# Optimization experiments

Measured on AMD Instinct MI355X. Metric: run time of the kernel, lower is better.

Reference implementation:

```python
import jax, jax.numpy as jnp
import numpy as np

DELTA_VAR = 0.5
DELTA_DIST = 1.5
ALPHA, BETA, GAMMA = 1.0, 1.0, 0.001
EPS = 1e-8


def setup_inputs() -> dict:
    key = jax.random.key(0)
    k1, k2 = jax.random.split(key)
    N, D, C = 4_000_000, 16, 64
    features = jax.random.normal(k1, (N, D), dtype=jnp.float32)
    labels = jax.random.randint(k2, (N,), 0, C)  # every cluster id present w.h.p.
    return {"features": features, "labels": labels, "num_clusters": C}


def _discriminative_loss(features, labels, C):
    # per-cluster counts and means (scatter-mean, replaces the boolean-mask loop)
    ones = jnp.ones(features.shape[0], dtype=features.dtype)
    counts = jax.ops.segment_sum(ones, labels, num_segments=C)            # (C,)
    sums = jax.ops.segment_sum(features, labels, num_segments=C)          # (C, D)
    safe_counts = jnp.maximum(counts, 1.0)
    means = sums / safe_counts[:, None]                                   # (C, D)

    # intra-cluster (variance) loss: mean over clusters of mean hinge^2
    dists = jnp.linalg.norm(features - means[labels] + EPS, axis=1)       # (N,)
    hinge2 = jnp.square(jnp.maximum(dists - DELTA_VAR, 0.0))
    per_cluster = jax.ops.segment_sum(hinge2, labels, num_segments=C) / safe_counts
    var_loss = jnp.mean(per_cluster)

    # inter-cluster (distance) loss over all ordered pairs i != j
    diff = means[:, None, :] - means[None, :, :] + EPS                    # (C, C, D)
    pdist = jnp.linalg.norm(diff, axis=-1)                                # (C, C)
    h = jnp.square(jnp.maximum(2.0 * DELTA_DIST - pdist, 0.0))
    h = h * (1.0 - jnp.eye(C, dtype=h.dtype))
    dist_loss = jnp.sum(h) / float(C * (C - 1))

    # regularization: mean centroid norm
    reg_loss = jnp.mean(jnp.linalg.norm(means + EPS, axis=1))

    total = ALPHA * var_loss + BETA * dist_loss + GAMMA * reg_loss
    return jnp.stack([total, var_loss, dist_loss, reg_loss])  # (4,)


def reference(features, labels, num_clusters):
    return _discriminative_loss(features, labels, num_clusters)
```

## Files before the change

kernel.cpp:

```cpp
#include <hip/hip_runtime.h>
#include <math.h>

#define C 64
#define D 16
#define EPSF 1e-8f
#define DVAR 0.5f
#define DDIST 1.5f
#define FPSCALE 65536.0f
#define INV_FPSCALE (1.0f / 65536.0f)
#define VARSCALE 4294967296.0
#define INV_VARSCALE (1.0 / 4294967296.0)

#define NB 2048
#define SLICE 1088

#define GF0 (NB * SLICE)
#define V0 (GF0 + 1088)

__global__ __launch_bounds__(256) void k_sums(const float4* __restrict__ f4,
                                              const int* __restrict__ labels, int N,
                                              int* __restrict__ arr) {
    __shared__ int s_sums[C * 17];
    __shared__ unsigned s_cnt[C];
    int t = threadIdx.x;
    int b = blockIdx.x;
    for (int i = t; i < C * 17; i += 256) s_sums[i] = 0;
    if (t < C) s_cnt[t] = 0u;
    __syncthreads();

    int ntiles = (N + 255) >> 8;
    for (int it = b; it < ntiles; it += NB) {
        int tile = ntiles - 1 - it;
        int p = (tile << 8) + t;
        if (p >= N) continue;
        int c = labels[p] & (C - 1);
        float4 a  = f4[4 * p + 0];
        float4 bb = f4[4 * p + 1];
        float4 cc = f4[4 * p + 2];
        float4 dd = f4[4 * p + 3];
        int* row = &s_sums[c * 17];
        atomicAdd(row + 0,  __float2int_rn(a.x  * FPSCALE));
        atomicAdd(row + 1,  __float2int_rn(a.y  * FPSCALE));
        atomicAdd(row + 2,  __float2int_rn(a.z  * FPSCALE));
        atomicAdd(row + 3,  __float2int_rn(a.w  * FPSCALE));
        atomicAdd(row + 4,  __float2int_rn(bb.x * FPSCALE));
        atomicAdd(row + 5,  __float2int_rn(bb.y * FPSCALE));
        atomicAdd(row + 6,  __float2int_rn(bb.z * FPSCALE));
        atomicAdd(row + 7,  __float2int_rn(bb.w * FPSCALE));
        atomicAdd(row + 8,  __float2int_rn(cc.x * FPSCALE));
        atomicAdd(row + 9,  __float2int_rn(cc.y * FPSCALE));
        atomicAdd(row + 10, __float2int_rn(cc.z * FPSCALE));
        atomicAdd(row + 11, __float2int_rn(cc.w * FPSCALE));
        atomicAdd(row + 12, __float2int_rn(dd.x * FPSCALE));
        atomicAdd(row + 13, __float2int_rn(dd.y * FPSCALE));
        atomicAdd(row + 14, __float2int_rn(dd.z * FPSCALE));
        atomicAdd(row + 15, __float2int_rn(dd.w * FPSCALE));
        atomicAdd(&s_cnt[c], 1u);
    }
    __syncthreads();
    for (int i = t; i < SLICE; i += 256) {
        int v = (i < C * D) ? s_sums[(i >> 4) * 17 + (i & 15)] : (int)s_cnt[i - C * D];
        arr[b * SLICE + i] = v;
    }
}

__global__ __launch_bounds__(256) void k_reduce(const int* __restrict__ arr,
                                                int* __restrict__ g_final) {
    __shared__ int s[256];
    int o = blockIdx.x;
    int t = threadIdx.x;
    int part = 0;
    #pragma unroll
    for (int j = 0; j < NB / 256; j++)
        part += arr[(t + j * 256) * SLICE + o];
    s[t] = part;
    __syncthreads();
    for (int st = 128; st > 0; st >>= 1) {
        if (t < st) s[t] += s[t + st];
        __syncthreads();
    }
    if (t == 0) g_final[o] = s[0];
}

__global__ __launch_bounds__(256) void k_hinge(const float4* __restrict__ f4,
                                               const int* __restrict__ labels, int N,
                                               const int* __restrict__ g_final,
                                               unsigned long long* __restrict__ g_var) {
    __shared__ __align__(16) float s_means[C * 20];
    __shared__ float s_w[C];
    __shared__ float s_red[256];
    int t = threadIdx.x;
    int b = blockIdx.x;
    for (int i = t; i < C * D; i += 256) {
        int c = i >> 4, d = i & 15;
        float cnt = fmaxf((float)g_final[C * D + c], 1.0f);
        s_means[c * 20 + d] = (float)g_final[i] * INV_FPSCALE / cnt;
    }
    if (t < C) s_w[t] = 1.0f / (fmaxf((float)g_final[C * D + t], 1.0f) * (float)C);
    __syncthreads();

    float acc = 0.0f;
    int gid = b * 256 + t;
    int stride = NB * 256;
    for (int p = gid; p < N; p += stride) {
        int c = labels[p] & (C - 1);
        const float* m = &s_means[c * 20];
        float4 m0 = *(const float4*)(m + 0);
        float4 m1 = *(const float4*)(m + 4);
        float4 m2 = *(const float4*)(m + 8);
        float4 m3 = *(const float4*)(m + 12);
        float4 a  = f4[4 * p + 0];
        float4 bb = f4[4 * p + 1];
        float4 cc = f4[4 * p + 2];
        float4 dd = f4[4 * p + 3];
        float ss = 0.0f, dx;
        dx = a.x - m0.x + EPSF; ss += dx * dx;
        dx = a.y - m0.y + EPSF; ss += dx * dx;
        dx = a.z - m0.z + EPSF; ss += dx * dx;
        dx = a.w - m0.w + EPSF; ss += dx * dx;
        dx = bb.x - m1.x + EPSF; ss += dx * dx;
        dx = bb.y - m1.y + EPSF; ss += dx * dx;
        dx = bb.z - m1.z + EPSF; ss += dx * dx;
        dx = bb.w - m1.w + EPSF; ss += dx * dx;
        dx = cc.x - m2.x + EPSF; ss += dx * dx;
        dx = cc.y - m2.y + EPSF; ss += dx * dx;
        dx = cc.z - m2.z + EPSF; ss += dx * dx;
        dx = cc.w - m2.w + EPSF; ss += dx * dx;
        dx = dd.x - m3.x + EPSF; ss += dx * dx;
        dx = dd.y - m3.y + EPSF; ss += dx * dx;
        dx = dd.z - m3.z + EPSF; ss += dx * dx;
        dx = dd.w - m3.w + EPSF; ss += dx * dx;
        float h = fmaxf(sqrtf(ss) - DVAR, 0.0f);
        acc += h * h * s_w[c];
    }
    s_red[t] = acc;
    __syncthreads();
    for (int s = 128; s > 0; s >>= 1) {
        if (t < s) s_red[t] += s_red[t + s];
        __syncthreads();
    }
    if (t == 0)
        g_var[b] = (unsigned long long)((double)s_red[0] * VARSCALE + 0.5);
}

__global__ __launch_bounds__(256) void k_final(const int* __restrict__ g_final,
                                               const unsigned long long* __restrict__ g_var,
                                               float* __restrict__ out) {
    __shared__ float s_m[C * 17];
    __shared__ float red[256];
    __shared__ unsigned long long red64[256];
    int t = threadIdx.x;
    for (int i = t; i < C * D; i += 256) {
        int c = i >> 4, d = i & 15;
        float cnt = fmaxf((float)g_final[C * D + c], 1.0f);
        s_m[c * 17 + d] = (float)g_final[i] * INV_FPSCALE / cnt;
    }
    unsigned long long vq = 0ull;
    #pragma unroll
    for (int j = 0; j < NB / 256; j++) vq += g_var[t + j * 256];
    red64[t] = vq;
    __syncthreads();
    for (int s = 128; s > 0; s >>= 1) {
        if (t < s) red64[t] += red64[t + s];
        __syncthreads();
    }
    float var_loss = (float)((double)red64[0] * INV_VARSCALE);
    __syncthreads();

    float ds = 0.0f;
    for (int p = t; p < C * C; p += 256) {
        int i = p >> 6, j = p & 63;
        if (i != j) {
            float ss = 0.0f;
            #pragma unroll
            for (int d = 0; d < D; d++) {
                float df = s_m[i * 17 + d] - s_m[j * 17 + d] + EPSF;
                ss += df * df;
            }
            float h = fmaxf(2.0f * DDIST - sqrtf(ss), 0.0f);
            ds += h * h;
        }
    }
    red[t] = ds;
    __syncthreads();
    for (int s = 128; s > 0; s >>= 1) {
        if (t < s) red[t] += red[t + s];
        __syncthreads();
    }
    float dist_loss = red[0] / (float)(C * (C - 1));
    __syncthreads();

    float rg = 0.0f;
    if (t < C) {
        float ss = 0.0f;
        #pragma unroll
        for (int d = 0; d < D; d++) {
            float m = s_m[t * 17 + d] + EPSF;
            ss += m * m;
        }
        rg = sqrtf(ss);
    }
    red[t] = rg;
    __syncthreads();
    for (int s = 128; s > 0; s >>= 1) {
        if (t < s) red[t] += red[t + s];
        __syncthreads();
    }
    float reg_loss = red[0] / (float)C;

    if (t == 0) {
        out[0] = var_loss + dist_loss + 0.001f * reg_loss;
        out[1] = var_loss;
        out[2] = dist_loss;
        out[3] = reg_loss;
    }
}

extern "C" void kernel_launch(void* const* d_in, const int* in_sizes, int n_in,
                              void* d_out, int out_size, void* d_ws, size_t ws_size,
                              hipStream_t stream) {
    const float4* f4 = (const float4*)d_in[0];
    const int* labels = (const int*)d_in[1];
    int N = in_sizes[0] / D;

    int* ws = (int*)d_ws;
    int* arr = ws;
    int* g_final = ws + GF0;
    unsigned long long* g_var = (unsigned long long*)(ws + V0);
    float* out = (float*)d_out;

    hipLaunchKernelGGL(k_sums, dim3(NB), dim3(256), 0, stream, f4, labels, N, arr);
    hipLaunchKernelGGL(k_reduce, dim3(SLICE), dim3(256), 0, stream, arr, g_final);
    hipLaunchKernelGGL(k_hinge, dim3(NB), dim3(256), 0, stream, f4, labels, N, g_final, g_var);
    hipLaunchKernelGGL(k_final, dim3(1), dim3(256), 0, stream, g_final, g_var, out);
}
```

Before: 420.0 us.

## Pack two fixed-point sums per 64-bit LDS atomic; unroll hinge loop by two

The per-cluster sum accumulation packs two biased 32-bit fixed-point values into one 64-bit shared-memory atomic, halving the number of LDS atomics per point. The bias is removed using the per-cluster count when writing partials. The tile loop now drops the per-iteration bounds check by handling the tail separately. The hinge kernel loads two points per iteration so more memory loads are in flight. The packing relies on per-block sums staying within the 32-bit halves without carrying across, which holds only for bounded feature magnitudes and per-block counts.

```diff
diff --git a/kernel.cpp b/kernel.cpp
--- a/kernel.cpp
+++ b/kernel.cpp
@@ -10,56 +10,82 @@
 #define INV_FPSCALE (1.0f / 65536.0f)
 #define VARSCALE 4294967296.0
 #define INV_VARSCALE (1.0 / 4294967296.0)
+#define BIAS 524288
 
 #define NB 2048
+#define NTHR (NB * 256)
 #define SLICE 1088
 
 #define GF0 (NB * SLICE)
 #define V0 (GF0 + 1088)
+
+__device__ __forceinline__ unsigned long long pack2(float x, float y) {
+    unsigned lo = (unsigned)(__float2int_rn(x * FPSCALE) + BIAS);
+    unsigned hi = (unsigned)(__float2int_rn(y * FPSCALE) + BIAS);
+    return ((unsigned long long)hi << 32) | (unsigned long long)lo;
+}
 
 __global__ __launch_bounds__(256) void k_sums(const float4* __restrict__ f4,
                                               const int* __restrict__ labels, int N,
                                               int* __restrict__ arr) {
-    __shared__ int s_sums[C * 17];
+    __shared__ unsigned long long s_sum2[C * 9];
     __shared__ unsigned s_cnt[C];
     int t = threadIdx.x;
     int b = blockIdx.x;
-    for (int i = t; i < C * 17; i += 256) s_sums[i] = 0;
+    for (int i = t; i < C * 9; i += 256) s_sum2[i] = 0ull;
     if (t < C) s_cnt[t] = 0u;
     __syncthreads();
 
-    int ntiles = (N + 255) >> 8;
-    for (int it = b; it < ntiles; it += NB) {
-        int tile = ntiles - 1 - it;
+    int nfull = N >> 8;
+    for (int it = b; it < nfull; it += NB) {
+        int tile = nfull - 1 - it;
         int p = (tile << 8) + t;
-        if (p >= N) continue;
         int c = labels[p] & (C - 1);
         float4 a  = f4[4 * p + 0];
         float4 bb = f4[4 * p + 1];
         float4 cc = f4[4 * p + 2];
         float4 dd = f4[4 * p + 3];
-        int* row = &s_sums[c * 17];
-        atomicAdd(row + 0,  __float2int_rn(a.x  * FPSCALE));
-        atomicAdd(row + 1,  __float2int_rn(a.y  * FPSCALE));
-        atomicAdd(row + 2,  __float2int_rn(a.z  * FPSCALE));
-        atomicAdd(row + 3,  __float2int_rn(a.w  * FPSCALE));
-        atomicAdd(row + 4,  __float2int_rn(bb.x * FPSCALE));
-        atomicAdd(row + 5,  __float2int_rn(bb.y * FPSCALE));
-        atomicAdd(row + 6,  __float2int_rn(bb.z * FPSCALE));
-        atomicAdd(row + 7,  __float2int_rn(bb.w * FPSCALE));
-        atomicAdd(row + 8,  __float2int_rn(cc.x * FPSCALE));
-        atomicAdd(row + 9,  __float2int_rn(cc.y * FPSCALE));
-        atomicAdd(row + 10, __float2int_rn(cc.z * FPSCALE));
-        atomicAdd(row + 11, __float2int_rn(cc.w * FPSCALE));
-        atomicAdd(row + 12, __float2int_rn(dd.x * FPSCALE));
-        atomicAdd(row + 13, __float2int_rn(dd.y * FPSCALE));
-        atomicAdd(row + 14, __float2int_rn(dd.z * FPSCALE));
-        atomicAdd(row + 15, __float2int_rn(dd.w * FPSCALE));
+        unsigned long long* row = &s_sum2[c * 9];
+        atomicAdd(row + 0, pack2(a.x,  a.y));
+        atomicAdd(row + 1, pack2(a.z,  a.w));
+        atomicAdd(row + 2, pack2(bb.x, bb.y));
+        atomicAdd(row + 3, pack2(bb.z, bb.w));
+        atomicAdd(row + 4, pack2(cc.x, cc.y));
+        atomicAdd(row + 5, pack2(cc.z, cc.w));
+        atomicAdd(row + 6, pack2(dd.x, dd.y));
+        atomicAdd(row + 7, pack2(dd.z, dd.w));
         atomicAdd(&s_cnt[c], 1u);
     }
+    int tail = N & 255;
+    if (tail && b == 0 && t < tail) {
+        int p = (nfull << 8) + t;
+        int c = labels[p] & (C - 1);
+        float4 a  = f4[4 * p + 0];
+        float4 bb = f4[4 * p + 1];
+        float4 cc = f4[4 * p + 2];
+        float4 dd = f4[4 * p + 3];
+        unsigned long long* row = &s_sum2[c * 9];
+        atomicAdd(row + 0, pack2(a.x,  a.y));
+        atomicAdd(row + 1, pack2(a.z,  a.w));
+        atomicAdd(row + 2, pack2(bb.x, bb.y));
+        atomicAdd(row + 3, pack2(bb.z, bb.w));
+        atomicAdd(row + 4, pack2(cc.x, cc.y));
+        atomicAdd(row + 5, pack2(cc.z, cc.w));
+        atomicAdd(row + 6, pack2(dd.x, dd.y));
+        atomicAdd(row + 7, pack2(dd.z, dd.w));
+        atomicAdd(&s_cnt[c], 1u);
+    }
     __syncthreads();
     for (int i = t; i < SLICE; i += 256) {
-        int v = (i < C * D) ? s_sums[(i >> 4) * 17 + (i & 15)] : (int)s_cnt[i - C * D];
+        int v;
+        if (i < C * D) {
+            int c = i >> 4, d = i & 15;
+            unsigned long long w = s_sum2[c * 9 + (d >> 1)];
+            unsigned half = (d & 1) ? (unsigned)(w >> 32) : (unsigned)w;
+            v = (int)(half - (s_cnt[c] << 19));
+        } else {
+            v = (int)s_cnt[i - C * D];
+        }
         arr[b * SLICE + i] = v;
     }
 }
@@ -80,6 +106,36 @@
         __syncthreads();
     }
     if (t == 0) g_final[o] = s[0];
+}
+
+__device__ __forceinline__ float point_term(const float* __restrict__ s_means,
+                                            const float* __restrict__ s_w,
+                                            float4 a, float4 bb, float4 cc, float4 dd,
+                                            int c) {
+    const float* m = &s_means[c * 20];
+    float4 m0 = *(const float4*)(m + 0);
+    float4 m1 = *(const float4*)(m + 4);
+    float4 m2 = *(const float4*)(m + 8);
+    float4 m3 = *(const float4*)(m + 12);
+    float ss = 0.0f, dx;
+    dx = a.x - m0.x + EPSF; ss += dx * dx;
+    dx = a.y - m0.y + EPSF; ss += dx * dx;
+    dx = a.z - m0.z + EPSF; ss += dx * dx;
+    dx = a.w - m0.w + EPSF; ss += dx * dx;
+    dx = bb.x - m1.x + EPSF; ss += dx * dx;
+    dx = bb.y - m1.y + EPSF; ss += dx * dx;
+    dx = bb.z - m1.z + EPSF; ss += dx * dx;
+    dx = bb.w - m1.w + EPSF; ss += dx * dx;
+    dx = cc.x - m2.x + EPSF; ss += dx * dx;
+    dx = cc.y - m2.y + EPSF; ss += dx * dx;
+    dx = cc.z - m2.z + EPSF; ss += dx * dx;
+    dx = cc.w - m2.w + EPSF; ss += dx * dx;
+    dx = dd.x - m3.x + EPSF; ss += dx * dx;
+    dx = dd.y - m3.y + EPSF; ss += dx * dx;
+    dx = dd.z - m3.z + EPSF; ss += dx * dx;
+    dx = dd.w - m3.w + EPSF; ss += dx * dx;
+    float h = fmaxf(sqrtf(ss) - DVAR, 0.0f);
+    return h * h * s_w[c];
 }
 
 __global__ __launch_bounds__(256) void k_hinge(const float4* __restrict__ f4,
@@ -99,39 +155,35 @@
     if (t < C) s_w[t] = 1.0f / (fmaxf((float)g_final[C * D + t], 1.0f) * (float)C);
     __syncthreads();
 
+    int gid = b * 256 + t;
+    int rounds = N >> 19;
+    int rem = N - (rounds << 19);
     float acc = 0.0f;
-    int gid = b * 256 + t;
-    int stride = NB * 256;
-    for (int p = gid; p < N; p += stride) {
-        int c = labels[p] & (C - 1);
-        const float* m = &s_means[c * 20];
-        float4 m0 = *(const float4*)(m + 0);
-        float4 m1 = *(const float4*)(m + 4);
-        float4 m2 = *(const float4*)(m + 8);
-        float4 m3 = *(const float4*)(m + 12);
-        float4 a  = f4[4 * p + 0];
-        float4 bb = f4[4 * p + 1];
-        float4 cc = f4[4 * p + 2];
-        float4 dd = f4[4 * p + 3];
-        float ss = 0.0f, dx;
-        dx = a.x - m0.x + EPSF; ss += dx * dx;
-        dx = a.y - m0.y + EPSF; ss += dx * dx;
-        dx = a.z - m0.z + EPSF; ss += dx * dx;
-        dx = a.w - m0.w + EPSF; ss += dx * dx;
-        dx = bb.x - m1.x + EPSF; ss += dx * dx;
-        dx = bb.y - m1.y + EPSF; ss += dx * dx;
-        dx = bb.z - m1.z + EPSF; ss += dx * dx;
-        dx = bb.w - m1.w + EPSF; ss += dx * dx;
-        dx = cc.x - m2.x + EPSF; ss += dx * dx;
-        dx = cc.y - m2.y + EPSF; ss += dx * dx;
-        dx = cc.z - m2.z + EPSF; ss += dx * dx;
-        dx = cc.w - m2.w + EPSF; ss += dx * dx;
-        dx = dd.x - m3.x + EPSF; ss += dx * dx;
-        dx = dd.y - m3.y + EPSF; ss += dx * dx;
-        dx = dd.z - m3.z + EPSF; ss += dx * dx;
-        dx = dd.w - m3.w + EPSF; ss += dx * dx;
-        float h = fmaxf(sqrtf(ss) - DVAR, 0.0f);
-        acc += h * h * s_w[c];
+    int p = gid;
+    for (int r = 0; r + 2 <= rounds; r += 2) {
+        int p0 = p, p1 = p + NTHR;
+        int c0 = labels[p0] & (C - 1);
+        int c1 = labels[p1] & (C - 1);
+        float4 a0 = f4[4 * p0 + 0], b0 = f4[4 * p0 + 1],
+               e0 = f4[4 * p0 + 2], d0 = f4[4 * p0 + 3];
+        float4 a1 = f4[4 * p1 + 0], b1 = f4[4 * p1 + 1],
+               e1 = f4[4 * p1 + 2], d1 = f4[4 * p1 + 3];
+        acc += point_term(s_means, s_w, a0, b0, e0, d0, c0);
+        acc += point_term(s_means, s_w, a1, b1, e1, d1, c1);
+        p += 2 * NTHR;
+    }
+    if (rounds & 1) {
+        int c0 = labels[p] & (C - 1);
+        float4 a0 = f4[4 * p + 0], b0 = f4[4 * p + 1],
+               e0 = f4[4 * p + 2], d0 = f4[4 * p + 3];
+        acc += point_term(s_means, s_w, a0, b0, e0, d0, c0);
+        p += NTHR;
+    }
+    if (gid < rem) {
+        int c0 = labels[p] & (C - 1);
+        float4 a0 = f4[4 * p + 0], b0 = f4[4 * p + 1],
+               e0 = f4[4 * p + 2], d0 = f4[4 * p + 3];
+        acc += point_term(s_means, s_w, a0, b0, e0, d0, c0);
     }
     s_red[t] = acc;
     __syncthreads();
```

Result: no change. 420.6 us (+0.1%).
